# Optimization experiments

Measured on AMD Instinct MI355X. Metric: run time of the kernel, lower is better.

Reference implementation:

```python
import math
import jax, jax.numpy as jnp
import numpy as np

G_RATIO = 0.5
TB_FACTOR = 1e-3


def _expand(x):
    # x: [B,H,W]; 3x3 all-ones-except-center neighbor conv (same filter for every sample)
    k = jnp.ones((1, 1, 3, 3), x.dtype).at[0, 0, 1, 1].set(0.0)
    y = jax.lax.conv_general_dilated(x[:, None], k, (1, 1), 'SAME')
    return y[:, 0]


def _st_softmax_noexp(val):
    # straight-through normalized selection over flattened map
    B = val.shape[0]
    v = val.reshape(B, -1)
    y = v / v.sum(-1, keepdims=True)
    ind = jnp.argmax(y, -1)
    y_hard = jax.nn.one_hot(ind, y.shape[-1], dtype=y.dtype)
    y = y + jax.lax.stop_gradient(y_hard - y)
    return y.reshape(val.shape)


def _heuristic(gm):
    # gm: [B,H,W] one-hot goal maps -> Chebyshev + tb*Euclidean distance field
    B, H, W = gm.shape
    loc = jnp.stack(jnp.meshgrid(jnp.arange(H), jnp.arange(W), indexing='ij'), 0).astype(gm.dtype)  # [2,H,W]
    loc_e = loc.reshape(2, -1)[None]                      # [1,2,HW]
    goal_loc = jnp.einsum('kij,bij->bk', loc, gm)[:, :, None]  # [B,2,1]
    d = jnp.abs(loc_e - goal_loc)                         # [B,2,HW]
    h = d.sum(1) - d.min(1)
    euc = jnp.sqrt(((loc_e - goal_loc) ** 2).sum(1))
    return (h + TB_FACTOR * euc).reshape(B, H, W)


def _forward_core(cost_maps, start_maps, goal_maps, obstacles_maps):
    cm, sm, gm, om = cost_maps[:, 0], start_maps[:, 0], goal_maps[:, 0], obstacles_maps[:, 0]
    B, H, W = cm.shape
    h = _heuristic(gm) + cm
    goal_idx = jnp.argmax(gm.reshape(B, -1), -1)
    parents0 = jnp.broadcast_to(goal_idx[:, None].astype(cm.dtype), (B, H * W))
    inv_sqrt = 1.0 / math.sqrt(W)
    Tmax = W * W

    def step(carry, i):
        g, open_m, hist, parents, done, t = carry
        f = G_RATIO * g + (1.0 - G_RATIO) * h
        f_exp = jnp.exp(-f * inv_sqrt) * open_m
        snm = _st_softmax_noexp(f_exp)
        dist = (snm * gm).sum((1, 2), keepdims=True)
        unsolved = (dist < 1e-8).astype(cm.dtype)
        hist_n = jnp.clip(hist + snm, 0.0, 1.0)
        open_n = jnp.clip(open_m - unsolved * snm, 0.0, 1.0)
        nb = _expand(snm) * om
        g2 = _expand((g + cm) * snm)
        idx = ((1.0 - open_n) * (1.0 - hist_n) + open_n * (g > g2).astype(cm.dtype)) * nb
        idx = jax.lax.stop_gradient(idx)
        g_n = jax.lax.stop_gradient(g2 * idx + g * (1.0 - idx))
        open_n = jax.lax.stop_gradient(jnp.clip(open_n + idx, 0.0, 1.0))
        idx_f = idx.reshape(B, -1)
        new_par = jnp.argmax(snm.reshape(B, -1), -1)[:, None].astype(cm.dtype)
        par_n = new_par * idx_f + parents * (1.0 - idx_f)
        done_n = jnp.all(unsolved == 0)
        sel = lambda new, old: jnp.where(done, old, new)  # emulate the torch early break
        carry_n = (sel(g_n, g), sel(open_n, open_m), sel(hist_n, hist), sel(par_n, parents),
                   jnp.logical_or(done, done_n), jnp.where(done, t, i))
        return carry_n, None

    init = (jnp.zeros_like(sm), sm, jnp.zeros_like(sm), parents0,
            jnp.array(False), jnp.array(0, jnp.int32))
    (g, open_m, hist, parents, done, t), _ = jax.lax.scan(
        step, init, jnp.arange(Tmax, dtype=jnp.int32))
    return hist[:, None], parents, t


def _backtrack(goal_maps, parents, t):
    gm = goal_maps[:, 0]
    B, H, W = gm.shape
    par_i = parents.astype(jnp.int32)
    goal_f = gm.reshape(B, -1).astype(jnp.int32)
    loc = (par_i * goal_f).sum(-1)
    rng = jnp.arange(B)

    def bt(i, val):
        path, loc = val
        path = path.at[rng, loc].set(1)
        loc = jnp.take_along_axis(par_i, loc[:, None], -1)[:, 0]
        return (path, loc)

    path, _ = jax.lax.fori_loop(0, t, bt, (goal_f, loc))
    return path.reshape(B, 1, H, W)


def setup_inputs() -> dict:
    key = jax.random.key(0)
    k1, k2, k3, k4 = jax.random.split(key, 4)
    B, H, W = 16, 32, 32
    cost_maps = jax.random.uniform(k1, (B, 1, H, W), dtype=jnp.float32)
    sidx = jax.random.randint(k2, (B,), 0, H * W)
    gidx = jax.random.randint(k3, (B,), 0, H * W)
    gidx = jnp.where(gidx == sidx, (gidx + 1) % (H * W), gidx)
    start_maps = jax.nn.one_hot(sidx, H * W, dtype=jnp.float32).reshape(B, 1, H, W)
    goal_maps = jax.nn.one_hot(gidx, H * W, dtype=jnp.float32).reshape(B, 1, H, W)
    obstacles_maps = (jax.random.uniform(k4, (B, 1, H, W)) > 0.05).astype(jnp.float32)
    obstacles_maps = jnp.clip(obstacles_maps + start_maps + goal_maps, 0.0, 1.0)
    return {'cost_maps': cost_maps, 'start_maps': start_maps,
            'goal_maps': goal_maps, 'obstacles_maps': obstacles_maps}


def reference(cost_maps, start_maps, goal_maps, obstacles_maps):
    histories, parents, t = _forward_core(cost_maps, start_maps, goal_maps, obstacles_maps)
    path_maps = _backtrack(goal_maps, parents, t)
    return histories, path_maps
```

## Files before the change

kernel.cpp:

```cpp
#include <hip/hip_runtime.h>
#include <math.h>

#define HW 1024
#define NB 16
#define TMAXS 1024

typedef unsigned long long ull;

__device__ __forceinline__ double u2d(ull u) {
  return __longlong_as_double((long long)u);
}
__device__ __forceinline__ ull d2u(double d) {
  return (ull)__double_as_longlong(d);
}

__device__ __forceinline__ float keyval(float g, float h) {
#pragma clang fp contract(off)
  const float INV = 0.17677669529663687f;
  float f = 0.5f * g + 0.5f * h;
  return expf(-f * INV);
}

template <int CTRL>
__device__ __forceinline__ double dpp_fmax64(double x) {
  ull u = d2u(x);
  int lo = (int)(unsigned)u;
  int hi = (int)(unsigned)(u >> 32);
  int lo2 = __builtin_amdgcn_update_dpp(0, lo, CTRL, 0xF, 0xF, false);
  int hi2 = __builtin_amdgcn_update_dpp(0, hi, CTRL, 0xF, 0xF, false);
  double y = u2d(((ull)(unsigned)hi2 << 32) | (unsigned)lo2);
  return fmax(x, y);
}

extern "C" __global__ void __launch_bounds__(64) astar_fused(
    const float* __restrict__ cm_g, const float* __restrict__ sm_g,
    const float* __restrict__ gm_g, const float* __restrict__ om_g,
    float* __restrict__ out) {
#pragma clang fp contract(off)
  const int b = blockIdx.x;
  const int lane = threadIdx.x;

  __shared__ __align__(16) ull key2[HW];
  __shared__ __align__(16) float4 gch[HW];
  __shared__ __align__(16) unsigned flg[HW];
  __shared__ __align__(16) unsigned par[HW];
  const float* gchf = (const float*)gch;

  const float* cm = cm_g + b * HW;
  const float* sm = sm_g + b * HW;
  const float* gm = gm_g + b * HW;
  const float* om = om_g + b * HW;

  float4 c4[4], o4[4];
  int gi = -1, si = -1;
#pragma unroll
  for (int q = 0; q < 4; ++q) {
    const int base = q * 256 + lane * 4;
    c4[q] = *(const float4*)(cm + base);
    o4[q] = *(const float4*)(om + base);
    const float4 s4 = *(const float4*)(sm + base);
    const float4 g4 = *(const float4*)(gm + base);
    const float sv[4] = {s4.x, s4.y, s4.z, s4.w};
    const float gv[4] = {g4.x, g4.y, g4.z, g4.w};
#pragma unroll
    for (int j = 0; j < 4; ++j) {
      if (gv[j] > 0.5f) gi = base + j;
      if (sv[j] > 0.5f) si = base + j;
    }
  }
#pragma unroll
  for (int m = 32; m >= 1; m >>= 1) {
    const int og = __shfl_xor(gi, m, 64);
    const int os = __shfl_xor(si, m, 64);
    gi = (og > gi) ? og : gi;
    si = (os > si) ? os : si;
  }
  const int goal = gi, start = si;

  const float grf = (float)(goal >> 5), gcf = (float)(goal & 31);
#pragma unroll
  for (int q = 0; q < 4; ++q) {
    const int base = q * 256 + lane * 4;
    const float cv[4] = {c4[q].x, c4[q].y, c4[q].z, c4[q].w};
    const float ov[4] = {o4[q].x, o4[q].y, o4[q].z, o4[q].w};
    ull pk[4];
    unsigned fv[4];
#pragma unroll
    for (int j = 0; j < 4; ++j) {
      const int cell = base + j;
      const float rr = (float)(cell >> 5), cc = (float)(cell & 31);
      const float dr = fabsf(rr - grf), dc = fabsf(cc - gcf);
      const float h0 = (dr + dc) - fminf(dr, dc);
      const float euc = sqrtf(dr * dr + dc * dc);
      const float t1 = 0.001f * euc;
      const float hh = h0 + t1;
      const float hf = hh + cv[j];
      gch[cell] = make_float4(0.0f, cv[j], cv[j], hf);
      fv[j] = (ov[j] > 0.5f) ? 1u : 0u;
      pk[j] = (ull)(1023 - cell);
      if (cell == start) {
        fv[j] |= 2u;
        pk[j] |= d2u((double)keyval(0.0f, hf));
      }
    }
    *(uint4*)&flg[base] = make_uint4(fv[0], fv[1], fv[2], fv[3]);
    *(uint4*)&par[base] =
        make_uint4((unsigned)goal, (unsigned)goal, (unsigned)goal, (unsigned)goal);
    ulonglong2 k01, k23;
    k01.x = pk[0]; k01.y = pk[1];
    k23.x = pk[2]; k23.y = pk[3];
    *(ulonglong2*)&key2[base] = k01;
    *(ulonglong2*)&key2[base + 2] = k23;
  }
  __builtin_amdgcn_wave_barrier();

  ulonglong2 r[8];
#pragma unroll
  for (int q = 0; q < 8; ++q)
    r[q] = *(const ulonglong2*)&key2[q * 128 + lane * 2];

  int dro = 0, dco = 0;
  if (lane < 8) {
    const int k = (lane < 4) ? lane : lane + 1;
    dro = k / 3 - 1;
    dco = k % 3 - 1;
  }

  int sel = start;
  bool reached = false;

#pragma unroll 1
  for (int step = 0; step < TMAXS; ++step) {
    if (sel == goal) { reached = true; break; }

    const float g2 = gchf[4 * sel + 2];
    int n = -1;
    unsigned f = 0;
    float4 v = make_float4(0.f, 0.f, 0.f, 0.f);
    if (lane < 8) {
      const int nr = (sel >> 5) + dro, nc = (sel & 31) + dco;
      if ((unsigned)nr < 32u && (unsigned)nc < 32u) {
        n = (nr << 5) | nc;
        f = flg[n];
        v = gch[n];
      }
    }
    unsigned fs = 0;
    if (lane == 8) fs = flg[sel];

    double m = 0.0;
#pragma unroll
    for (int q = 0; q < 8; ++q) {
      const int base = q * 128 + lane * 2;
      const ull a = (base == sel) ? (ull)(1023 - base) : r[q].x;
      const ull c = (base + 1 == sel) ? (ull)(1022 - base) : r[q].y;
      m = fmax(m, fmax(u2d(a), u2d(c)));
    }

    if (lane < 8 && n >= 0) {
      const bool upd =
          (f & 1u) && (((f & 6u) == 0u) || (((f & 2u) != 0u) && (v.x > g2)));
      if (upd) {
        gch[n] = make_float4(g2, v.y, g2 + v.y, v.w);
        flg[n] = f | 2u;
        par[n] = (unsigned)sel;
        const ull pk = d2u((double)keyval(g2, v.w)) | (ull)(1023 - n);
        key2[n] = pk;
        m = fmax(m, u2d(pk));
      }
    }
    if (lane == 8) {
      flg[sel] = (fs | 4u) & ~2u;
      key2[sel] = (ull)(1023 - sel);
    }
    __builtin_amdgcn_wave_barrier();

#pragma unroll
    for (int q = 0; q < 8; ++q)
      r[q] = *(const ulonglong2*)&key2[q * 128 + lane * 2];

    m = dpp_fmax64<0x111>(m);
    m = dpp_fmax64<0x112>(m);
    m = dpp_fmax64<0x114>(m);
    m = dpp_fmax64<0x118>(m);
    m = dpp_fmax64<0x142>(m);
    m = dpp_fmax64<0x143>(m);
    const int lo63 = __builtin_amdgcn_readlane((int)(unsigned)d2u(m), 63);
    sel = 1023 - (lo63 & 1023);
  }
  if (reached && lane == 0) flg[goal] |= 4u;
  __builtin_amdgcn_wave_barrier();

  if (lane == 0) {
    const unsigned pv = par[goal];
    par[goal] = pv | 0x80000000u;
    unsigned loc = pv & 1023u;
#pragma unroll 1
    for (int i = 0; i < HW; ++i) {
      const unsigned w = par[loc];
      if (w & 0x80000000u) break;
      par[loc] = w | 0x80000000u;
      loc = w & 1023u;
    }
  }
  __builtin_amdgcn_wave_barrier();

#pragma unroll
  for (int q = 0; q < 4; ++q) {
    const int base = q * 256 + lane * 4;
    float4 hv, pv;
    hv.x = (flg[base + 0] & 4u) ? 1.0f : 0.0f;
    hv.y = (flg[base + 1] & 4u) ? 1.0f : 0.0f;
    hv.z = (flg[base + 2] & 4u) ? 1.0f : 0.0f;
    hv.w = (flg[base + 3] & 4u) ? 1.0f : 0.0f;
    pv.x = (par[base + 0] >> 31) ? 1.0f : 0.0f;
    pv.y = (par[base + 1] >> 31) ? 1.0f : 0.0f;
    pv.z = (par[base + 2] >> 31) ? 1.0f : 0.0f;
    pv.w = (par[base + 3] >> 31) ? 1.0f : 0.0f;
    *(float4*)(out + b * HW + base) = hv;
    *(float4*)(out + NB * HW + b * HW + base) = pv;
  }
}

extern "C" void kernel_launch(void* const* d_in, const int* in_sizes, int n_in,
                              void* d_out, int out_size, void* d_ws,
                              size_t ws_size, hipStream_t stream) {
  const float* cm = (const float*)d_in[0];
  const float* sm = (const float*)d_in[1];
  const float* gm = (const float*)d_in[2];
  const float* om = (const float*)d_in[3];
  float* out = (float*)d_out;
  hipLaunchKernelGGL(astar_fused, dim3(NB), dim3(64), 0, stream, cm, sm, gm,
                     om, out);
}
```

Measured before the change: 78.40 us.

## Replace full 1024-key register scan with two-level group-max index

Replaces the per-step scan of all 1024 packed keys held in registers (16 keys per lane) with a two-level structure: a 64-entry shared array holding the maximum key of each 16-cell group. Each step, 16 lanes recompute the selected cell's group maximum while updated neighbours raise their group entries with shared-memory atomicMax. The wave then reduces only one value per lane. This removes the per-step reload of 8 ulonglong2 from LDS and the 16-way compare, at the cost of LDS 64-bit atomics and a more intricate ordering of the stale values.

New measurement: 77.63 us. Within noise of the previous version (-1.0%).

```diff
diff --git a/kernel.cpp b/kernel.cpp
--- a/kernel.cpp
+++ b/kernel.cpp
@@ -44,6 +44,7 @@
   __shared__ __align__(16) float4 gch[HW];
   __shared__ __align__(16) unsigned flg[HW];
   __shared__ __align__(16) unsigned par[HW];
+  __shared__ __align__(16) ull level1[64];
   const float* gchf = (const float*)gch;
 
   const float* cm = cm_g + b * HW;
@@ -77,6 +78,7 @@
   }
   const int goal = gi, start = si;
 
+  level1[lane] = 0ull;
   const float grf = (float)(goal >> 5), gcf = (float)(goal & 31);
 #pragma unroll
   for (int q = 0; q < 4; ++q) {
@@ -102,6 +104,7 @@
         fv[j] |= 2u;
         pk[j] |= d2u((double)keyval(0.0f, hf));
       }
+      atomicMax(&level1[cell >> 4], pk[j]);
     }
     *(uint4*)&flg[base] = make_uint4(fv[0], fv[1], fv[2], fv[3]);
     *(uint4*)&par[base] =
@@ -113,11 +116,7 @@
     *(ulonglong2*)&key2[base + 2] = k23;
   }
   __builtin_amdgcn_wave_barrier();
-
-  ulonglong2 r[8];
-#pragma unroll
-  for (int q = 0; q < 8; ++q)
-    r[q] = *(const ulonglong2*)&key2[q * 128 + lane * 2];
+  ull stale = level1[lane];
 
   int dro = 0, dco = 0;
   if (lane < 8) {
@@ -132,61 +131,61 @@
 #pragma unroll 1
   for (int step = 0; step < TMAXS; ++step) {
     if (sel == goal) { reached = true; break; }
-
+    const int gp = sel >> 4;
+
+    if (lane == 8) level1[gp] = 0ull;
     const float g2 = gchf[4 * sel + 2];
     int n = -1;
-    unsigned f = 0;
-    float4 v = make_float4(0.f, 0.f, 0.f, 0.f);
     if (lane < 8) {
       const int nr = (sel >> 5) + dro, nc = (sel & 31) + dco;
-      if ((unsigned)nr < 32u && (unsigned)nc < 32u) {
-        n = (nr << 5) | nc;
-        f = flg[n];
-        v = gch[n];
-      }
-    }
-    unsigned fs = 0;
-    if (lane == 8) fs = flg[sel];
-
-    double m = 0.0;
-#pragma unroll
-    for (int q = 0; q < 8; ++q) {
-      const int base = q * 128 + lane * 2;
-      const ull a = (base == sel) ? (ull)(1023 - base) : r[q].x;
-      const ull c = (base + 1 == sel) ? (ull)(1022 - base) : r[q].y;
-      m = fmax(m, fmax(u2d(a), u2d(c)));
-    }
-
+      if ((unsigned)nr < 32u && (unsigned)nc < 32u) n = (nr << 5) | nc;
+    } else if (lane == 8) {
+      n = sel;
+    }
+    unsigned f = 0;
+    if (n >= 0) f = flg[n];
+    float4 v = make_float4(0.f, 0.f, 0.f, 0.f);
+    if (lane < 8 && n >= 0) v = gch[n];
+    ull gc = 0ull;
+    const bool grpLane = (lane >= 32) && (lane < 48);
+    if (grpLane) {
+      const int gcell = gp * 16 + (lane - 32);
+      gc = key2[gcell];
+      if (gcell == sel) gc = (ull)(1023 - sel);
+      atomicMax(&level1[gp], gc);
+    }
+
+    bool updv = false;
+    ull pk = 0ull;
     if (lane < 8 && n >= 0) {
-      const bool upd =
-          (f & 1u) && (((f & 6u) == 0u) || (((f & 2u) != 0u) && (v.x > g2)));
-      if (upd) {
-        gch[n] = make_float4(g2, v.y, g2 + v.y, v.w);
-        flg[n] = f | 2u;
-        par[n] = (unsigned)sel;
-        const ull pk = d2u((double)keyval(g2, v.w)) | (ull)(1023 - n);
-        key2[n] = pk;
-        m = fmax(m, u2d(pk));
-      }
-    }
-    if (lane == 8) {
-      flg[sel] = (fs | 4u) & ~2u;
-      key2[sel] = (ull)(1023 - sel);
-    }
-    __builtin_amdgcn_wave_barrier();
-
-#pragma unroll
-    for (int q = 0; q < 8; ++q)
-      r[q] = *(const ulonglong2*)&key2[q * 128 + lane * 2];
-
+      updv = (f & 1u) && (((f & 6u) == 0u) || (((f & 2u) != 0u) && (v.x > g2)));
+      if (updv) pk = d2u((double)keyval(g2, v.w)) | (ull)(1023 - n);
+    }
+    if (updv) {
+      gch[n] = make_float4(g2, v.y, g2 + v.y, v.w);
+      par[n] = (unsigned)sel;
+    }
+    if (updv || lane == 8) {
+      flg[n] = (lane == 8) ? ((f | 4u) & ~2u) : (f | 2u);
+      key2[n] = (lane == 8) ? (ull)(1023 - sel) : pk;
+    }
+    if (updv) atomicMax(&level1[n >> 4], pk);
+
+    double m = (lane == gp) ? 0.0 : u2d(stale);
+    if (grpLane) m = fmax(m, u2d(gc));
+    if (updv) m = fmax(m, u2d(pk));
     m = dpp_fmax64<0x111>(m);
     m = dpp_fmax64<0x112>(m);
     m = dpp_fmax64<0x114>(m);
     m = dpp_fmax64<0x118>(m);
     m = dpp_fmax64<0x142>(m);
     m = dpp_fmax64<0x143>(m);
+
+    stale = level1[lane];
+
     const int lo63 = __builtin_amdgcn_readlane((int)(unsigned)d2u(m), 63);
     sel = 1023 - (lo63 & 1023);
+    __builtin_amdgcn_wave_barrier();
   }
   if (reached && lane == 0) flg[goal] |= 4u;
   __builtin_amdgcn_wave_barrier();
```
